# Kernel tuning notes

Measured on AMD Instinct MI355X. Metric: run time of the kernel, lower is better.

The kernel has to match this reference:

```python
import jax, jax.numpy as jnp
import numpy as np

S, B, D, H = 2048, 2, 1024, 16
DK = D // H  # 64

def setup_inputs() -> dict:
    key = jax.random.key(0)
    ks = jax.random.split(key, 11)
    scale = 1.0 / np.sqrt(D)
    return {
        "query": jax.random.normal(ks[0], (S, B, D), dtype=jnp.float32),
        "key":   jax.random.normal(ks[1], (S, B, D), dtype=jnp.float32),
        "value": jax.random.normal(ks[2], (S, B, D), dtype=jnp.float32),
        "Wq": jax.random.normal(ks[3], (D, D), dtype=jnp.float32) * scale,
        "bq": jax.random.normal(ks[4], (D,), dtype=jnp.float32) * scale,
        "Wk": jax.random.normal(ks[5], (D, D), dtype=jnp.float32) * scale,
        "bk": jax.random.normal(ks[6], (D,), dtype=jnp.float32) * scale,
        "Wv": jax.random.normal(ks[7], (D, D), dtype=jnp.float32) * scale,
        "bv": jax.random.normal(ks[8], (D,), dtype=jnp.float32) * scale,
        "Wo": jax.random.normal(ks[9], (D, D), dtype=jnp.float32) * scale,
        "bo": jax.random.normal(ks[10], (D,), dtype=jnp.float32) * scale,
    }

def _split_heads(x):
    # [S, B, D] -> [H, B, S, DK]  (matches .view(S,B,H,DK).transpose(0,2))
    return x.reshape(S, B, H, DK).transpose(2, 1, 0, 3)

def reference(query, key, value, Wq, bq, Wk, bk, Wv, bv, Wo, bo):
    q = _split_heads(query @ Wq.T + bq)
    k = _split_heads(key   @ Wk.T + bk)
    v = _split_heads(value @ Wv.T + bv)
    scores = jnp.einsum('hbqd,hbkd->hbqk', q, k) / jnp.sqrt(jnp.float32(DK))
    align = jax.nn.softmax(scores, axis=-1)
    x = jnp.einsum('hbqk,hbkd->hbqd', align, v)  # [H,B,S,DK]
    x = x.transpose(2, 1, 0, 3).reshape(S, B, D)  # back to [S,B,D]
    return x @ Wo.T + bo
```

## Files before the change

### kernel.cpp

```cpp
#include <hip/hip_runtime.h>
#include <math.h>

#define SS 2048
#define BB 2
#define DD 1024
#define HH 16
#define DKK 64
#define MM (SS*BB)

typedef _Float16 f16;
typedef __attribute__((ext_vector_type(8))) _Float16 f16x8;
typedef __attribute__((ext_vector_type(2))) __fp16 fp16x2r;
typedef __attribute__((ext_vector_type(4))) float f32x4;
typedef __attribute__((ext_vector_type(16))) float f32x16;

__device__ __forceinline__ unsigned pk2(float a, float b) {
    union { fp16x2r h; unsigned u; } v;
    v.h = __builtin_amdgcn_cvt_pkrtz(a, b);
    return v.u;
}
__device__ __forceinline__ void gload_lds16(const void* g, void* l) {
    __builtin_amdgcn_global_load_lds(
        (const __attribute__((address_space(1))) unsigned*)g,
        (__attribute__((address_space(3))) unsigned*)l, 16, 0, 0);
}

__global__ __launch_bounds__(256)
void cvt_all(const float* __restrict__ q, const float* __restrict__ k,
             const float* __restrict__ v, const float* __restrict__ wq,
             const float* __restrict__ wk, const float* __restrict__ wv,
             const float* __restrict__ wo,
             f16* __restrict__ xout, f16* __restrict__ wout)
{
    const int z = blockIdx.y;
    const float* src;
    f16* dst;
    if (z < 3) {
        src = z == 0 ? q : (z == 1 ? k : v);
        dst = xout + (size_t)z*MM*DD;
    } else {
        if (blockIdx.x >= DD*DD/8/256) return;
        src = z == 3 ? wq : (z == 4 ? wk : (z == 5 ? wv : wo));
        dst = wout + (size_t)(z-3)*DD*DD;
    }
    size_t t = (size_t)blockIdx.x*256 + threadIdx.x;
    float4 f0 = ((const float4*)src)[t*2];
    float4 f1 = ((const float4*)src)[t*2+1];
    uint4 r;
    r.x = pk2(f0.x, f0.y); r.y = pk2(f0.z, f0.w);
    r.z = pk2(f1.x, f1.y); r.w = pk2(f1.z, f1.w);
    ((uint4*)dst)[t] = r;
}

__global__ __launch_bounds__(256)
void qkv_gemm(const f16* __restrict__ A16, const f16* __restrict__ W16,
              const float* __restrict__ bq, const float* __restrict__ bk,
              const float* __restrict__ bv,
              f16* __restrict__ Qh, f16* __restrict__ Kh, f16* __restrict__ Vt)
{
    __shared__ __align__(16) f16 As[128*32];
    __shared__ __align__(16) f16 Bs[128*32];

    const int tid  = threadIdx.x;
    const int w    = tid >> 6;
    const int lane = tid & 63;
    const int ln   = lane & 15;
    const int quad = lane >> 4;
    const int z  = blockIdx.z;
    const int m0 = blockIdx.x * 128;
    const int n0 = blockIdx.y * 128;
    const int wm = (w >> 1) * 64;
    const int wn = (w & 1) * 64;

    const f16* A = A16 + (size_t)z*MM*DD;
    const f16* W = W16 + (size_t)z*DD*DD;
    const float* bias = z == 0 ? bq : (z == 1 ? bk : bv);

    f32x4 acc[4][4];
    #pragma unroll
    for (int mt = 0; mt < 4; mt++)
        #pragma unroll
        for (int nt = 0; nt < 4; nt++)
            acc[mt][nt] = (f32x4){0.f,0.f,0.f,0.f};

    int slot[2], r_[2], gch[2];
    #pragma unroll
    for (int i = 0; i < 2; i++) {
        slot[i] = i*256 + tid;
        r_[i]   = slot[i] >> 2;
        gch[i]  = ((slot[i] & 3) ^ ((r_[i] >> 1) & 3)) * 8;
    }

    for (int step = 0; step < DD/32; step++) {
        const int k0 = step*32;
        __syncthreads();
        #pragma unroll
        for (int i = 0; i < 2; i++) {
            gload_lds16(A + (size_t)(m0 + r_[i])*DD + k0 + gch[i],
                        (char*)As + slot[i]*16);
            gload_lds16(W + (size_t)(n0 + r_[i])*DD + k0 + gch[i],
                        (char*)Bs + slot[i]*16);
        }
        __syncthreads();

        f16x8 af[4], bf[4];
        #pragma unroll
        for (int mt = 0; mt < 4; mt++) {
            int r = wm + mt*16 + ln;
            af[mt] = *(const f16x8*)&As[r*32 + ((quad ^ ((r>>1)&3)) << 3)];
        }
        #pragma unroll
        for (int nt = 0; nt < 4; nt++) {
            int r = wn + nt*16 + ln;
            bf[nt] = *(const f16x8*)&Bs[r*32 + ((quad ^ ((r>>1)&3)) << 3)];
        }
        #pragma unroll
        for (int mt = 0; mt < 4; mt++)
            #pragma unroll
            for (int nt = 0; nt < 4; nt++)
                acc[mt][nt] = __builtin_amdgcn_mfma_f32_16x16x32_f16(
                    af[mt], bf[nt], acc[mt][nt], 0, 0, 0);
    }

    float bvv[4];
    #pragma unroll
    for (int nt = 0; nt < 4; nt++) bvv[nt] = bias[n0 + wn + nt*16 + ln];

    if (z == 2) {
        #pragma unroll
        for (int mt = 0; mt < 4; mt++) {
            int mbase = m0 + wm + mt*16 + quad*4;
            int s0 = mbase >> 1;
            #pragma unroll
            for (int nt = 0; nt < 4; nt++) {
                int n = n0 + wn + nt*16 + ln;
                int h = n >> 6, d = n & 63;
                float v0 = acc[mt][nt][0] + bvv[nt];
                float v1 = acc[mt][nt][1] + bvv[nt];
                float v2 = acc[mt][nt][2] + bvv[nt];
                float v3 = acc[mt][nt][3] + bvv[nt];
                *(unsigned*)&Vt[((size_t)(0*HH + h)*DKK + d)*SS + s0] = pk2(v0, v2);
                *(unsigned*)&Vt[((size_t)(1*HH + h)*DKK + d)*SS + s0] = pk2(v1, v3);
            }
        }
    } else {
        const float scale = z == 0 ? 0.125f : 1.0f;
        f16* dst = z == 0 ? Qh : Kh;
        #pragma unroll
        for (int mt = 0; mt < 4; mt++)
            #pragma unroll
            for (int nt = 0; nt < 4; nt++)
                #pragma unroll
                for (int r = 0; r < 4; r++) {
                    int m = m0 + wm + mt*16 + quad*4 + r;
                    int n = n0 + wn + nt*16 + ln;
                    int s = m >> 1, b = m & 1;
                    int h = n >> 6, d = n & 63;
                    dst[(((size_t)(b*HH + h))*SS + s)*DKK + d] =
                        (f16)((acc[mt][nt][r] + bvv[nt]) * scale);
                }
    }
}

__global__ __launch_bounds__(256)
void out_gemm(const f16* __restrict__ A, const f16* __restrict__ W,
              const float* __restrict__ bias, float* __restrict__ out)
{
    __shared__ __align__(16) f16 As[64*32];
    __shared__ __align__(16) f16 Bs[128*32];

    const int tid  = threadIdx.x;
    const int w    = tid >> 6;
    const int lane = tid & 63;
    const int ln   = lane & 15;
    const int quad = lane >> 4;
    const int m0 = blockIdx.x * 64;
    const int n0 = blockIdx.y * 128;
    const int wm = (w >> 1) * 32;
    const int wn = (w & 1) * 64;

    f32x4 acc[2][4];
    #pragma unroll
    for (int mt = 0; mt < 2; mt++)
        #pragma unroll
        for (int nt = 0; nt < 4; nt++)
            acc[mt][nt] = (f32x4){0.f,0.f,0.f,0.f};

    const int rA  = tid >> 2;
    const int gchA = ((tid & 3) ^ ((rA >> 1) & 3)) * 8;
    int slotB[2], rB[2], gchB[2];
    #pragma unroll
    for (int i = 0; i < 2; i++) {
        slotB[i] = i*256 + tid;
        rB[i]    = slotB[i] >> 2;
        gchB[i]  = ((slotB[i] & 3) ^ ((rB[i] >> 1) & 3)) * 8;
    }

    for (int step = 0; step < DD/32; step++) {
        const int k0 = step*32;
        __syncthreads();
        gload_lds16(A + (size_t)(m0 + rA)*DD + k0 + gchA, (char*)As + tid*16);
        #pragma unroll
        for (int i = 0; i < 2; i++)
            gload_lds16(W + (size_t)(n0 + rB[i])*DD + k0 + gchB[i],
                        (char*)Bs + slotB[i]*16);
        __syncthreads();

        f16x8 af[2], bf[4];
        #pragma unroll
        for (int mt = 0; mt < 2; mt++) {
            int r = wm + mt*16 + ln;
            af[mt] = *(const f16x8*)&As[r*32 + ((quad ^ ((r>>1)&3)) << 3)];
        }
        #pragma unroll
        for (int nt = 0; nt < 4; nt++) {
            int r = wn + nt*16 + ln;
            bf[nt] = *(const f16x8*)&Bs[r*32 + ((quad ^ ((r>>1)&3)) << 3)];
        }
        #pragma unroll
        for (int mt = 0; mt < 2; mt++)
            #pragma unroll
            for (int nt = 0; nt < 4; nt++)
                acc[mt][nt] = __builtin_amdgcn_mfma_f32_16x16x32_f16(
                    af[mt], bf[nt], acc[mt][nt], 0, 0, 0);
    }

    #pragma unroll
    for (int nt = 0; nt < 4; nt++) {
        float bvv = bias[n0 + wn + nt*16 + ln];
        #pragma unroll
        for (int mt = 0; mt < 2; mt++)
            #pragma unroll
            for (int r = 0; r < 4; r++) {
                int m = m0 + wm + mt*16 + quad*4 + r;
                int n = n0 + wn + nt*16 + ln;
                out[(size_t)m*DD + n] = acc[mt][nt][r] + bvv;
            }
    }
}

__global__ __launch_bounds__(512, 4)
void attn_v6(const f16* __restrict__ Q, const f16* __restrict__ K,
             const f16* __restrict__ V, f16* __restrict__ Xh)
{
    __shared__ __align__(16) char arena[67584];
    f16*   const PlBase = (f16*)(arena + 32768);
    float* const Ol     = (float*)(arena + 32768);
    float* const Ls     = (float*)(arena + 66048);

    const int tid  = threadIdx.x;
    const int g    = tid >> 8;
    const int wg   = tid >> 6;
    const int w4   = wg & 3;
    const int lane = tid & 63;
    const int l5   = lane & 31;
    const int hf   = lane >> 5;
    const int h = blockIdx.y, b = blockIdx.z;
    const size_t base = ((size_t)(b*HH + h)) * SS * DKK;
    const int Q0 = blockIdx.x * 128;
    const int q  = w4*32 + l5;

    f16x8 qf[4];
    #pragma unroll
    for (int ks = 0; ks < 4; ks++)
        qf[ks] = *(const f16x8*)(Q + base + (size_t)(Q0 + q)*DKK + ks*16 + hf*8);

    f16x8 ones;
    #pragma unroll
    for (int i = 0; i < 8; i++) ones[i] = (f16)1.0f;

    f32x16 o[2];
    o[0] = (f32x16)(0.f); o[1] = (f32x16)(0.f);
    f32x16 lacc = (f32x16)(0.f);

    const f16* const Ksg = (const f16*)(arena + g*8192);
    const f16* const Vsg = (const f16*)(arena + 16384 + g*8192);
    f16* const myP = PlBase + wg*2176 + l5*68;

    for (int t = 0; t < 16; t++) {
        __syncthreads();
        #pragma unroll
        for (int i = 0; i < 4; i++) {
            int slot = i*512 + tid;
            int kv   = slot >> 10;
            int s    = (slot >> 9) & 1;
            int idx  = slot & 511;
            int r    = idx >> 3, c8 = idx & 7;
            int kts  = s*16 + t;
            const f16* src = kv == 0
                ? K + base + (size_t)(kts*64 + r)*DKK + ((c8 ^ (r&7)) << 3)
                : V + base + (size_t)r*SS + kts*64 + ((c8 ^ (r&7)) << 3);
            gload_lds16(src, arena + kv*16384 + s*8192 + idx*16);
        }
        __syncthreads();

        f32x16 sc[2];
        sc[0] = (f32x16)(0.f); sc[1] = (f32x16)(0.f);
        #pragma unroll
        for (int ks = 0; ks < 4; ks++) {
            const int cc = ks*2 + hf;
            #pragma unroll
            for (int mt = 0; mt < 2; mt++) {
                int key = mt*32 + l5;
                f16x8 ka = *(const f16x8*)&Ksg[key*64 + ((cc ^ (key&7)) << 3)];
                sc[mt] = __builtin_amdgcn_mfma_f32_32x32x16_f16(ka, qf[ks], sc[mt], 0, 0, 0);
            }
        }

        #pragma unroll
        for (int mt = 0; mt < 2; mt++)
            #pragma unroll
            for (int gg = 0; gg < 4; gg++) {
                uint2 pk;
                pk.x = pk2(__expf(sc[mt][gg*4+0]), __expf(sc[mt][gg*4+1]));
                pk.y = pk2(__expf(sc[mt][gg*4+2]), __expf(sc[mt][gg*4+3]));
                *(uint2*)&myP[mt*32 + gg*8 + hf*4] = pk;
            }

        #pragma unroll
        for (int ks = 0; ks < 4; ks++) {
            union { uint2 u[2]; f16x8 v; } pbu;
            pbu.u[0] = *(const uint2*)&myP[ks*16 + hf*8];
            pbu.u[1] = *(const uint2*)&myP[ks*16 + hf*8 + 4];
            f16x8 pb = pbu.v;
            lacc = __builtin_amdgcn_mfma_f32_32x32x16_f16(ones, pb, lacc, 0, 0, 0);
            const int cc = ks*2 + hf;
            #pragma unroll
            for (int mt = 0; mt < 2; mt++) {
                int d = mt*32 + l5;
                f16x8 va = *(const f16x8*)&Vsg[d*64 + ((cc ^ (d&7)) << 3)];
                o[mt] = __builtin_amdgcn_mfma_f32_32x32x16_f16(va, pb, o[mt], 0, 0, 0);
            }
        }
    }

    __syncthreads();
    if (g == 1) {
        #pragma unroll
        for (int mt = 0; mt < 2; mt++)
            #pragma unroll
            for (int reg = 0; reg < 16; reg++) {
                int d = mt*32 + (reg & 3) + 8*(reg >> 2) + 4*hf;
                Ol[q*65 + d] = o[mt][reg];
            }
        if (hf == 0) Ls[q] = lacc[0];
    }
    __syncthreads();
    if (g == 0) {
        const float inv = 1.0f / (lacc[0] + Ls[q]);
        const int qg = Q0 + q;
        f16* xp = Xh + ((size_t)qg*BB + b)*DD + h*DKK;
        #pragma unroll
        for (int mt = 0; mt < 2; mt++)
            #pragma unroll
            for (int gg = 0; gg < 4; gg++) {
                float v0 = (o[mt][gg*4+0] + Ol[q*65 + mt*32 + 8*gg + 4*hf + 0]) * inv;
                float v1 = (o[mt][gg*4+1] + Ol[q*65 + mt*32 + 8*gg + 4*hf + 1]) * inv;
                float v2 = (o[mt][gg*4+2] + Ol[q*65 + mt*32 + 8*gg + 4*hf + 2]) * inv;
                float v3 = (o[mt][gg*4+3] + Ol[q*65 + mt*32 + 8*gg + 4*hf + 3]) * inv;
                uint2 pk;
                pk.x = pk2(v0, v1);
                pk.y = pk2(v2, v3);
                *(uint2*)&xp[mt*32 + gg*8 + hf*4] = pk;
            }
    }
}

extern "C" void kernel_launch(void* const* d_in, const int* in_sizes, int n_in,
                              void* d_out, int out_size, void* d_ws, size_t ws_size,
                              hipStream_t stream) {
    (void)in_sizes; (void)n_in; (void)out_size; (void)ws_size;
    const float* query = (const float*)d_in[0];
    const float* key   = (const float*)d_in[1];
    const float* value = (const float*)d_in[2];
    const float* Wq = (const float*)d_in[3];
    const float* bq = (const float*)d_in[4];
    const float* Wk = (const float*)d_in[5];
    const float* bk = (const float*)d_in[6];
    const float* Wv = (const float*)d_in[7];
    const float* bv = (const float*)d_in[8];
    const float* Wo = (const float*)d_in[9];
    const float* bo = (const float*)d_in[10];

    char* ws = (char*)d_ws;
    f16* A16 = (f16*)ws;
    f16* W16 = (f16*)(ws + 25165824);
    f16* Qh  = (f16*)(ws + 33554432);
    f16* Kh  = (f16*)(ws + 41943040);
    f16* Vt  = (f16*)(ws + 50331648);
    f16* Xh  = (f16*)(ws + 58720256);

    cvt_all<<<dim3(MM*DD/8/256, 7), 256, 0, stream>>>(
        query, key, value, Wq, Wk, Wv, Wo, A16, W16);

    qkv_gemm<<<dim3(MM/128, DD/128, 3), 256, 0, stream>>>(
        A16, W16, bq, bk, bv, Qh, Kh, Vt);

    attn_v6<<<dim3(SS/128, HH, BB), 512, 0, stream>>>(Qh, Kh, Vt, Xh);

    out_gemm<<<dim3(MM/64, DD/128), 256, 0, stream>>>(
        Xh, W16 + (size_t)3*DD*DD, bo, (float*)d_out);
}
```

Baseline: 227.9 us.

## Keep softmax probabilities in registers via lane shuffles and stage V transpose in LDS

The attention kernel no longer round-trips the exponentiated scores through shared memory. The P fragments are rearranged between half-waves with shuffles, and the row sum is accumulated with fdot2 instead of an extra MFMA against a ones vector. Shared memory drops to about 33 KB and the occupancy hint rises to 6, so more blocks can fit per CU. Separately, the V-projection epilogue transposes through LDS so that Vt gets 16-byte coalesced stores instead of scattered 4-byte ones, at the cost of extra barriers.

```diff
diff --git a/kernel.cpp b/kernel.cpp
--- a/kernel.cpp
+++ b/kernel.cpp
@@ -58,8 +58,10 @@
               const float* __restrict__ bv,
               f16* __restrict__ Qh, f16* __restrict__ Kh, f16* __restrict__ Vt)
 {
-    __shared__ __align__(16) f16 As[128*32];
-    __shared__ __align__(16) f16 Bs[128*32];
+    __shared__ __align__(16) char qsmem[16896];
+    f16* const As = (f16*)qsmem;
+    f16* const Bs = (f16*)(qsmem + 8192);
+    f16* const Ct = (f16*)qsmem;
 
     const int tid  = threadIdx.x;
     const int w    = tid >> 6;
@@ -128,19 +130,37 @@
 
     if (z == 2) {
         #pragma unroll
-        for (int mt = 0; mt < 4; mt++) {
-            int mbase = m0 + wm + mt*16 + quad*4;
-            int s0 = mbase >> 1;
-            #pragma unroll
-            for (int nt = 0; nt < 4; nt++) {
-                int n = n0 + wn + nt*16 + ln;
-                int h = n >> 6, d = n & 63;
-                float v0 = acc[mt][nt][0] + bvv[nt];
-                float v1 = acc[mt][nt][1] + bvv[nt];
-                float v2 = acc[mt][nt][2] + bvv[nt];
-                float v3 = acc[mt][nt][3] + bvv[nt];
-                *(unsigned*)&Vt[((size_t)(0*HH + h)*DKK + d)*SS + s0] = pk2(v0, v2);
-                *(unsigned*)&Vt[((size_t)(1*HH + h)*DKK + d)*SS + s0] = pk2(v1, v3);
+        for (int half = 0; half < 2; half++) {
+            __syncthreads();
+            if ((wn >> 6) == half) {
+                #pragma unroll
+                for (int mt = 0; mt < 4; mt++)
+                    #pragma unroll
+                    for (int nt = 0; nt < 4; nt++)
+                        #pragma unroll
+                        for (int r = 0; r < 4; r++) {
+                            int d = nt*16 + ln;
+                            int sl = (wm >> 1) + mt*8 + quad*2 + (r >> 1);
+                            Ct[d*132 + (r&1)*64 + sl] =
+                                (f16)(acc[mt][nt][r] + bvv[nt]);
+                        }
+            }
+            __syncthreads();
+            {
+                int d   = tid >> 2;
+                int bb2 = (tid >> 1) & 1;
+                int seg = tid & 1;
+                int hh  = (n0 >> 6) + half;
+                const f16* srcp = &Ct[d*132 + bb2*64 + seg*32];
+                f16* dstp = Vt + ((size_t)(bb2*HH + hh)*DKK + d)*SS
+                               + (m0 >> 1) + seg*32;
+                #pragma unroll
+                for (int k2 = 0; k2 < 4; k2++) {
+                    uint2 a = *(const uint2*)(srcp + k2*8);
+                    uint2 c = *(const uint2*)(srcp + k2*8 + 4);
+                    uint4 u; u.x = a.x; u.y = a.y; u.z = c.x; u.w = c.y;
+                    *(uint4*)(dstp + k2*8) = u;
+                }
             }
         }
     } else {
@@ -239,14 +259,13 @@
     }
 }
 
-__global__ __launch_bounds__(512, 4)
-void attn_v6(const f16* __restrict__ Q, const f16* __restrict__ K,
+__global__ __launch_bounds__(512, 6)
+void attn_v7(const f16* __restrict__ Q, const f16* __restrict__ K,
              const f16* __restrict__ V, f16* __restrict__ Xh)
 {
-    __shared__ __align__(16) char arena[67584];
-    f16*   const PlBase = (f16*)(arena + 32768);
-    float* const Ol     = (float*)(arena + 32768);
-    float* const Ls     = (float*)(arena + 66048);
+    __shared__ __align__(16) char arena[33792];
+    float* const Ol = (float*)arena;
+    float* const Ls = (float*)(arena + 33280);
 
     const int tid  = threadIdx.x;
     const int g    = tid >> 8;
@@ -265,17 +284,13 @@
     for (int ks = 0; ks < 4; ks++)
         qf[ks] = *(const f16x8*)(Q + base + (size_t)(Q0 + q)*DKK + ks*16 + hf*8);
 
-    f16x8 ones;
-    #pragma unroll
-    for (int i = 0; i < 8; i++) ones[i] = (f16)1.0f;
-
     f32x16 o[2];
     o[0] = (f32x16)(0.f); o[1] = (f32x16)(0.f);
-    f32x16 lacc = (f32x16)(0.f);
+    float lsum = 0.f;
+    fp16x2r one2; one2[0] = (__fp16)1.0f; one2[1] = (__fp16)1.0f;
 
     const f16* const Ksg = (const f16*)(arena + g*8192);
     const f16* const Vsg = (const f16*)(arena + 16384 + g*8192);
-    f16* const myP = PlBase + wg*2176 + l5*68;
 
     for (int t = 0; t < 16; t++) {
         __syncthreads();
@@ -294,36 +309,46 @@
         }
         __syncthreads();
 
-        f32x16 sc[2];
-        sc[0] = (f32x16)(0.f); sc[1] = (f32x16)(0.f);
-        #pragma unroll
-        for (int ks = 0; ks < 4; ks++) {
-            const int cc = ks*2 + hf;
-            #pragma unroll
-            for (int mt = 0; mt < 2; mt++) {
+        unsigned U[2][4][2];
+        #pragma unroll
+        for (int mt = 0; mt < 2; mt++) {
+            f32x16 sc = (f32x16)(0.f);
+            #pragma unroll
+            for (int ks = 0; ks < 4; ks++) {
+                const int cc = ks*2 + hf;
                 int key = mt*32 + l5;
                 f16x8 ka = *(const f16x8*)&Ksg[key*64 + ((cc ^ (key&7)) << 3)];
-                sc[mt] = __builtin_amdgcn_mfma_f32_32x32x16_f16(ka, qf[ks], sc[mt], 0, 0, 0);
-            }
-        }
-
-        #pragma unroll
-        for (int mt = 0; mt < 2; mt++)
+                sc = __builtin_amdgcn_mfma_f32_32x32x16_f16(ka, qf[ks], sc, 0, 0, 0);
+            }
             #pragma unroll
             for (int gg = 0; gg < 4; gg++) {
-                uint2 pk;
-                pk.x = pk2(__expf(sc[mt][gg*4+0]), __expf(sc[mt][gg*4+1]));
-                pk.y = pk2(__expf(sc[mt][gg*4+2]), __expf(sc[mt][gg*4+3]));
-                *(uint2*)&myP[mt*32 + gg*8 + hf*4] = pk;
-            }
+                unsigned u0 = pk2(__expf(sc[gg*4+0]), __expf(sc[gg*4+1]));
+                unsigned u1 = pk2(__expf(sc[gg*4+2]), __expf(sc[gg*4+3]));
+                U[mt][gg][0] = u0;
+                U[mt][gg][1] = u1;
+                union { unsigned u; fp16x2r h; } c0, c1;
+                c0.u = u0; c1.u = u1;
+                lsum = __builtin_amdgcn_fdot2(c0.h, one2, lsum, false);
+                lsum = __builtin_amdgcn_fdot2(c1.h, one2, lsum, false);
+            }
+        }
 
         #pragma unroll
         for (int ks = 0; ks < 4; ks++) {
-            union { uint2 u[2]; f16x8 v; } pbu;
-            pbu.u[0] = *(const uint2*)&myP[ks*16 + hf*8];
-            pbu.u[1] = *(const uint2*)&myP[ks*16 + hf*8 + 4];
+            const int mt0 = ks >> 1;
+            const int e   = (ks & 1) * 2;
+            unsigned k0 = hf ? U[mt0][e+1][0] : U[mt0][e][0];
+            unsigned k1 = hf ? U[mt0][e+1][1] : U[mt0][e][1];
+            unsigned s0 = hf ? U[mt0][e][0]   : U[mt0][e+1][0];
+            unsigned s1 = hf ? U[mt0][e][1]   : U[mt0][e+1][1];
+            unsigned r0 = __shfl_xor(s0, 32, 64);
+            unsigned r1 = __shfl_xor(s1, 32, 64);
+            union { unsigned u[4]; f16x8 v; } pbu;
+            pbu.u[0] = hf ? r0 : k0;
+            pbu.u[1] = hf ? r1 : k1;
+            pbu.u[2] = hf ? k0 : r0;
+            pbu.u[3] = hf ? k1 : r1;
             f16x8 pb = pbu.v;
-            lacc = __builtin_amdgcn_mfma_f32_32x32x16_f16(ones, pb, lacc, 0, 0, 0);
             const int cc = ks*2 + hf;
             #pragma unroll
             for (int mt = 0; mt < 2; mt++) {
@@ -334,6 +359,8 @@
         }
     }
 
+    float lfull = lsum + __shfl_xor(lsum, 32, 64);
+
     __syncthreads();
     if (g == 1) {
         #pragma unroll
@@ -343,11 +370,11 @@
                 int d = mt*32 + (reg & 3) + 8*(reg >> 2) + 4*hf;
                 Ol[q*65 + d] = o[mt][reg];
             }
-        if (hf == 0) Ls[q] = lacc[0];
+        if (hf == 0) Ls[q] = lfull;
     }
     __syncthreads();
     if (g == 0) {
-        const float inv = 1.0f / (lacc[0] + Ls[q]);
+        const float inv = 1.0f / (lfull + Ls[q]);
         const int qg = Q0 + q;
         f16* xp = Xh + ((size_t)qg*BB + b)*DD + h*DKK;
         #pragma unroll
@@ -396,7 +423,7 @@
     qkv_gemm<<<dim3(MM/128, DD/128, 3), 256, 0, stream>>>(
         A16, W16, bq, bk, bv, Qh, Kh, Vt);
 
-    attn_v6<<<dim3(SS/128, HH, BB), 512, 0, stream>>>(Qh, Kh, Vt, Xh);
+    attn_v7<<<dim3(SS/128, HH, BB), 512, 0, stream>>>(Qh, Kh, Vt, Xh);
 
     out_gemm<<<dim3(MM/64, DD/128), 256, 0, stream>>>(
         Xh, W16 + (size_t)3*DD*DD, bo, (float*)d_out);
```

New measurement: 258.1 us. 13.3% more time.
